# Kernel tuning notes

Hardware: AMD Instinct MI355X
Metric: run time of the kernel (lower is better)

The kernel has to match this reference:

```python
import jax, jax.numpy as jnp
import numpy as np

SIZE = 256


def setup_inputs() -> dict:
    key = jax.random.key(0)
    ks = jax.random.split(key, 16)
    B, T, S, V = 16, 128, 512, 32000
    s = SIZE
    inp = {}
    inp["inputs"] = jax.random.randint(ks[0], (B, T), 0, V)
    inp["features"] = jax.random.normal(ks[1], (B, S, 2 * s), dtype=jnp.float32)
    # parameters (PyTorch-style: y = x @ W.T + b)
    inp["emb"] = jax.random.normal(ks[2], (V, s), dtype=jnp.float32)
    inp["W_ih"] = jax.random.normal(ks[3], (4 * s, 2 * s), dtype=jnp.float32) * 0.05
    inp["W_hh"] = jax.random.normal(ks[4], (4 * s, s), dtype=jnp.float32) * 0.05
    inp["b_ih"] = jax.random.normal(ks[5], (4 * s,), dtype=jnp.float32) * 0.05
    inp["b_hh"] = jax.random.normal(ks[6], (4 * s,), dtype=jnp.float32) * 0.05
    inp["Wq"] = jax.random.normal(ks[7], (s, s), dtype=jnp.float32) * 0.05
    inp["bq"] = jax.random.normal(ks[8], (s,), dtype=jnp.float32) * 0.05
    inp["Wk"] = jax.random.normal(ks[9], (s, 2 * s), dtype=jnp.float32) * 0.05
    inp["bk"] = jax.random.normal(ks[10], (s,), dtype=jnp.float32) * 0.05
    inp["Wv"] = jax.random.normal(ks[11], (s, 2 * s), dtype=jnp.float32) * 0.05
    inp["bv"] = jax.random.normal(ks[12], (s,), dtype=jnp.float32) * 0.05
    inp["Wo"] = jax.random.normal(ks[13], (V, 2 * s), dtype=jnp.float32) * 0.05
    inp["bo"] = jax.random.normal(ks[14], (V,), dtype=jnp.float32) * 0.05
    return inp


def _decode(inputs, features, emb, W_ih, W_hh, b_ih, b_hh,
            Wq, bq, Wk, bk, Wv, bv, Wo, bo):
    B, T = inputs.shape
    s = emb.shape[1]
    embeddings = emb[inputs]                      # [B, T, s]
    # features are constant across timesteps -> hoist key/value projections
    keys = features @ Wk.T + bk                   # [B, S, s]
    values = features @ Wv.T + bv                 # [B, S, s]

    def step(carry, emb_t):
        h, c, context = carry
        x = jnp.concatenate([emb_t, context], axis=1)          # [B, 2s]
        gates = x @ W_ih.T + b_ih + h @ W_hh.T + b_hh          # [B, 4s]
        i, f, g, o = jnp.split(gates, 4, axis=1)               # PyTorch gate order
        i, f, o = jax.nn.sigmoid(i), jax.nn.sigmoid(f), jax.nn.sigmoid(o)
        g = jnp.tanh(g)
        c_new = f * c + i * g
        h_new = o * jnp.tanh(c_new)
        # attention
        query = h_new @ Wq.T + bq                              # [B, s]
        scores = jnp.einsum('bsd,bd->bs', keys, query)         # [B, S]
        weights = jax.nn.softmax(scores, axis=1)
        ctx = jnp.einsum('bsd,bs->bd', values, weights)        # [B, s]
        out = jnp.concatenate([h_new, ctx], axis=1) @ Wo.T + bo  # [B, V]
        return (h_new, c_new, ctx), out

    h0 = jnp.zeros((B, s), dtype=embeddings.dtype)
    c0 = jnp.zeros((B, s), dtype=embeddings.dtype)
    ctx0 = jnp.zeros((B, s), dtype=embeddings.dtype)
    _, outs = jax.lax.scan(step, (h0, c0, ctx0), jnp.swapaxes(embeddings, 0, 1))
    return jnp.swapaxes(outs, 0, 1)               # [B, T, V]


def reference(inputs, features, emb, W_ih, W_hh, b_ih, b_hh,
              Wq, bq, Wk, bk, Wv, bv, Wo, bo):
    return _decode(inputs, features, emb, W_ih, W_hh, b_ih, b_hh,
                   Wq, bq, Wk, bk, Wv, bv, Wo, bo)
```

## Files before the change

kernel.cpp:

```cpp
#include <hip/hip_runtime.h>
#include <hip/hip_fp16.h>

#define DEVI __device__ __forceinline__

typedef __attribute__((ext_vector_type(4))) float f32x4;
typedef __attribute__((ext_vector_type(8))) short bf16x8;
typedef __attribute__((ext_vector_type(8))) _Float16 f16x8;
typedef __attribute__((ext_vector_type(2))) _Float16 f16x2;
typedef unsigned long long ull;

DEVI ushort f2bf(float x) {
  union { float f; unsigned u; } v; v.f = x;
  unsigned r = v.u + 0x7fffu + ((v.u >> 16) & 1u);
  return (ushort)(r >> 16);
}
DEVI float bf2f(ushort b) {
  union { unsigned u; float f; } v; v.u = ((unsigned)b) << 16; return v.f;
}
DEVI unsigned packh2(float a, float b) {
  return ((unsigned)__half_as_ushort(__float2half(b)) << 16) |
         (unsigned)__half_as_ushort(__float2half(a));
}
DEVI float dot2(unsigned a, unsigned b, float c) {
#if __has_builtin(__builtin_amdgcn_fdot2)
  return __builtin_amdgcn_fdot2(__builtin_bit_cast(f16x2, a),
                                __builtin_bit_cast(f16x2, b), c, false);
#else
  f16x2 ha = __builtin_bit_cast(f16x2, a), hb = __builtin_bit_cast(f16x2, b);
  return c + (float)ha[0] * (float)hb[0] + (float)ha[1] * (float)hb[1];
#endif
}
DEVI float sigmoidf_(float x) { return 1.f / (1.f + __expf(-x)); }
DEVI float tanh_fast(float x) {
  float e = __expf(2.f * x);
  return 1.f - 2.f / (e + 1.f);
}

DEVI void gstore64(ull* p, ull v) {
  __hip_atomic_store(p, v, __ATOMIC_RELAXED, __HIP_MEMORY_SCOPE_AGENT);
}
DEVI ull gload64(const ull* p) {
  return __hip_atomic_load(p, __ATOMIC_RELAXED, __HIP_MEMORY_SCOPE_AGENT);
}

template<bool SPLIT, bool ABF16, bool BBF16>
__global__ __launch_bounds__(256)
void gemm_kernel(const void* __restrict__ A_, int lda, const int* __restrict__ Aidx,
                 const void* __restrict__ Bw_, int ldb,
                 const float* __restrict__ bias, float* __restrict__ C,
                 int N, int K)
{
  constexpr int BK  = SPLIT ? 32 : 64;
  constexpr int LDT = BK + 8;
  constexpr int NV  = (128 * BK / 4) / 256;

  __shared__ ushort Ah[128 * LDT];
  __shared__ ushort Bh[128 * LDT];
  __shared__ ushort Al[SPLIT ? 128 * LDT : 4];
  __shared__ ushort Bl[SPLIT ? 128 * LDT : 4];

  const int tid  = threadIdx.x;
  const int bm   = blockIdx.x * 128, bn = blockIdx.y * 128;
  const int lane = tid & 63, wave = tid >> 6;
  const int wr   = wave >> 1, wc = wave & 1;
  const int fr   = lane & 15, quad = lane >> 4;

  f32x4 acc[4][4] = {};

  for (int kt = 0; kt < K; kt += BK) {
    __syncthreads();
#pragma unroll
    for (int i = 0; i < NV; ++i) {
      int v   = i * 256 + tid;
      int row = v / (BK / 4);
      int c4  = (v % (BK / 4)) * 4;
      int arow = Aidx ? Aidx[bm + row] : (bm + row);
      if (ABF16) {
        const ushort* A = (const ushort*)A_;
        ushort4 h = *reinterpret_cast<const ushort4*>(A + (size_t)arow * lda + kt + c4);
        *reinterpret_cast<ushort4*>(&Ah[row * LDT + c4]) = h;
      } else {
        const float* A = (const float*)A_;
        const float4 x = *reinterpret_cast<const float4*>(A + (size_t)arow * lda + kt + c4);
        ushort4 h; h.x = f2bf(x.x); h.y = f2bf(x.y); h.z = f2bf(x.z); h.w = f2bf(x.w);
        *reinterpret_cast<ushort4*>(&Ah[row * LDT + c4]) = h;
        if (SPLIT) {
          ushort4 l;
          l.x = f2bf(x.x - bf2f(h.x)); l.y = f2bf(x.y - bf2f(h.y));
          l.z = f2bf(x.z - bf2f(h.z)); l.w = f2bf(x.w - bf2f(h.w));
          *reinterpret_cast<ushort4*>(&Al[row * LDT + c4]) = l;
        }
      }
    }
#pragma unroll
    for (int i = 0; i < NV; ++i) {
      int v   = i * 256 + tid;
      int row = v / (BK / 4);
      int c4  = (v % (BK / 4)) * 4;
      if (BBF16) {
        const ushort* B16 = (const ushort*)Bw_;
        ushort4 h = *reinterpret_cast<const ushort4*>(B16 + (size_t)(bn + row) * ldb + kt + c4);
        *reinterpret_cast<ushort4*>(&Bh[row * LDT + c4]) = h;
      } else {
        const float* Bw = (const float*)Bw_;
        const float4 x = *reinterpret_cast<const float4*>(Bw + (size_t)(bn + row) * ldb + kt + c4);
        ushort4 h; h.x = f2bf(x.x); h.y = f2bf(x.y); h.z = f2bf(x.z); h.w = f2bf(x.w);
        *reinterpret_cast<ushort4*>(&Bh[row * LDT + c4]) = h;
        if (SPLIT) {
          ushort4 l;
          l.x = f2bf(x.x - bf2f(h.x)); l.y = f2bf(x.y - bf2f(h.y));
          l.z = f2bf(x.z - bf2f(h.z)); l.w = f2bf(x.w - bf2f(h.w));
          *reinterpret_cast<ushort4*>(&Bl[row * LDT + c4]) = l;
        }
      }
    }
    __syncthreads();
#pragma unroll
    for (int ks = 0; ks < BK; ks += 32) {
      bf16x8 ah[4], bh[4];
#pragma unroll
      for (int i = 0; i < 4; ++i) {
        ah[i] = *reinterpret_cast<const bf16x8*>(&Ah[(wr * 64 + i * 16 + fr) * LDT + ks + quad * 8]);
        bh[i] = *reinterpret_cast<const bf16x8*>(&Bh[(wc * 64 + i * 16 + fr) * LDT + ks + quad * 8]);
      }
      if (SPLIT) {
        bf16x8 al[4], bl[4];
#pragma unroll
        for (int i = 0; i < 4; ++i) {
          al[i] = *reinterpret_cast<const bf16x8*>(&Al[(wr * 64 + i * 16 + fr) * LDT + ks + quad * 8]);
          bl[i] = *reinterpret_cast<const bf16x8*>(&Bl[(wc * 64 + i * 16 + fr) * LDT + ks + quad * 8]);
        }
#pragma unroll
        for (int i = 0; i < 4; ++i)
#pragma unroll
          for (int j = 0; j < 4; ++j) {
            acc[i][j] = __builtin_amdgcn_mfma_f32_16x16x32_bf16(ah[i], bh[j], acc[i][j], 0, 0, 0);
            acc[i][j] = __builtin_amdgcn_mfma_f32_16x16x32_bf16(ah[i], bl[j], acc[i][j], 0, 0, 0);
            acc[i][j] = __builtin_amdgcn_mfma_f32_16x16x32_bf16(al[i], bh[j], acc[i][j], 0, 0, 0);
          }
      } else {
#pragma unroll
        for (int i = 0; i < 4; ++i)
#pragma unroll
          for (int j = 0; j < 4; ++j)
            acc[i][j] = __builtin_amdgcn_mfma_f32_16x16x32_bf16(ah[i], bh[j], acc[i][j], 0, 0, 0);
      }
    }
  }
#pragma unroll
  for (int i = 0; i < 4; ++i)
#pragma unroll
    for (int j = 0; j < 4; ++j)
#pragma unroll
      for (int r = 0; r < 4; ++r) {
        int m = bm + wr * 64 + i * 16 + quad * 4 + r;
        int n = bn + wc * 64 + j * 16 + fr;
        float vv = acc[i][j][r];
        if (bias) vv += bias[n];
        C[(size_t)m * N + n] = vv;
      }
}

__global__ void prep_kernel(const float* __restrict__ Wq, float* __restrict__ WqT,
                            const float* __restrict__ b_ih, const float* __restrict__ b_hh,
                            float* __restrict__ bsum)
{
  int idx = blockIdx.x * 256 + threadIdx.x;
  if (idx < 65536) {
    int e = idx >> 8, d = idx & 255;
    WqT[idx] = Wq[d * 256 + e];
  } else if (idx < 66560) {
    int n = idx - 65536;
    bsum[n] = b_ih[n] + b_hh[n];
  }
}

__global__ void sb_kernel(const float* __restrict__ keys, const float* __restrict__ bq,
                          float* __restrict__ sb)
{
  int row  = blockIdx.x * 4 + (threadIdx.x >> 6);
  int lane = threadIdx.x & 63;
  const float* kr = keys + (size_t)row * 256;
  float acc = kr[lane] * bq[lane] + kr[64 + lane] * bq[64 + lane]
            + kr[128 + lane] * bq[128 + lane] + kr[192 + lane] * bq[192 + lane];
#pragma unroll
  for (int off = 1; off < 64; off <<= 1) acc += __shfl_xor(acc, off);
  if (lane == 0) sb[row] = acc;
}

__global__ void cvt_kernel(const float* __restrict__ src, ushort* __restrict__ dst, int n4)
{
  int i = blockIdx.x * 256 + threadIdx.x;
  if (i < n4) {
    float4 x = reinterpret_cast<const float4*>(src)[i];
    ushort4 h; h.x = f2bf(x.x); h.y = f2bf(x.y); h.z = f2bf(x.z); h.w = f2bf(x.w);
    reinterpret_cast<ushort4*>(dst)[i] = h;
  }
}

struct ScanSmem2 {
  unsigned k2p[64][131];
  unsigned vtp[256][35];
  unsigned xw[288];
  unsigned psp[32];
  float Erow[128];
  float gout[128];
  float ml[8][2];
  float cpart[4][128][2];
  float sc[8][64];
  float sbs[64];
};

DEVI int xwi(int w) { return (w >> 6) * 72 + (w & 63); }

__global__ __launch_bounds__(512, 1)
void scan2_kernel(const float* __restrict__ E, const float* __restrict__ K2g,
                  const float* __restrict__ sbg, const float* __restrict__ valg,
                  const float* __restrict__ W_ih, const float* __restrict__ W_hh,
                  ushort* __restrict__ hcb16,
                  ull* __restrict__ Hx,
                  ull* __restrict__ Px)
{
  extern __shared__ char smraw[];
  ScanSmem2& sm = *reinterpret_cast<ScanSmem2*>(smraw);
  const int g = blockIdx.x, tid = threadIdx.x;
  const int b = g >> 3, ss = g & 7;

  for (int idx = tid; idx < 64 * 128; idx += 512) {
    int j = idx >> 7, i = idx & 127;
    const float* src = K2g + (size_t)(b * 512 + ss * 64 + j) * 256 + 2 * i;
    sm.k2p[j][i] = packh2(src[0], src[1]);
  }
  for (int idx = tid; idx < 256 * 32; idx += 512) {
    int e = idx >> 5, jp = idx & 31;
    float v0 = valg[(size_t)(b * 512 + ss * 64 + 2 * jp) * 256 + e];
    float v1 = valg[(size_t)(b * 512 + ss * 64 + 2 * jp + 1) * 256 + e];
    sm.vtp[e][jp] = packh2(v0, v1);
  }
  if (tid < 64) sm.sbs[tid] = sbg[b * 512 + ss * 64 + tid];
  for (int i = tid; i < 288; i += 512) sm.xw[i] = 0;

  const int r  = tid >> 2, h4 = tid & 3;
  const int grow = (r >> 5) * 256 + ss * 32 + (r & 31);
  const float* wsrc = (h4 < 2)
      ? (W_ih + (size_t)grow * 512 + 256 + h4 * 128)
      : (W_hh + (size_t)grow * 256 + (h4 - 2) * 128);
  unsigned wreg[64];
#pragma unroll
  for (int i = 0; i < 32; ++i) {
    float4 w4 = reinterpret_cast<const float4*>(wsrc)[i];
    wreg[2 * i]     = packh2(w4.x, w4.y);
    wreg[2 * i + 1] = packh2(w4.z, w4.w);
  }

  float c_reg = 0.f;
  __syncthreads();

  const size_t hxb = (size_t)b * 128;
  const size_t pxb = (size_t)b * (8 * 130);

  for (int t = 0; t <= 128; ++t) {
    float epf = 0.f;
    if (t < 128 && tid < 128)
      epf = E[(size_t)(b * 128 + t) * 1024 + (tid >> 5) * 256 + ss * 32 + (tid & 31)];

    float accg = 0.f;
    if (t > 0) {
      const unsigned tag = (unsigned)t;
      const ull* PxP = Px + (size_t)((t - 1) & 1) * (16 * 8 * 130) + pxb;
      const int e2 = tid & 127, q = tid >> 7;
      const ull* p1 = &PxP[(2 * q) * 130 + e2];
      const ull* p2 = &PxP[(2 * q + 1) * 130 + e2];
      ull w1 = gload64(p1), w2 = gload64(p2);
      const ull* pm = &PxP[(tid >> 1) * 130 + 128 + (tid & 1)];
      ull wm = (tid < 16) ? gload64(pm) : 0;

      if (h4 >= 2) {
        const unsigned* xsrc = sm.xw + h4 * 72;
#pragma unroll
        for (int i = 0; i < 16; ++i) {
          uint4 xv = *reinterpret_cast<const uint4*>(xsrc + 4 * i);
          accg = dot2(wreg[4 * i + 0], xv.x, accg);
          accg = dot2(wreg[4 * i + 1], xv.y, accg);
          accg = dot2(wreg[4 * i + 2], xv.z, accg);
          accg = dot2(wreg[4 * i + 3], xv.w, accg);
        }
      }

      if (tid < 16) {
        while ((unsigned)(wm >> 32) != tag) { __builtin_amdgcn_s_sleep(1); wm = gload64(pm); }
        sm.ml[tid >> 1][tid & 1] = __uint_as_float((unsigned)wm);
      }
      while ((unsigned)(w1 >> 32) != tag) { __builtin_amdgcn_s_sleep(1); w1 = gload64(p1); }
      while ((unsigned)(w2 >> 32) != tag) { __builtin_amdgcn_s_sleep(1); w2 = gload64(p2); }
      __syncthreads();
      float M = sm.ml[0][0];
#pragma unroll
      for (int s3 = 1; s3 < 8; ++s3) M = fmaxf(M, sm.ml[s3][0]);
      float L = 0.f;
#pragma unroll
      for (int s3 = 0; s3 < 8; ++s3) L += sm.ml[s3][1] * __expf(sm.ml[s3][0] - M);
      float rcpL = 1.f / L;
      float wf0 = __expf(sm.ml[2 * q][0] - M);
      float wf1 = __expf(sm.ml[2 * q + 1][0] - M);
      f16x2 x1 = __builtin_bit_cast(f16x2, (unsigned)w1);
      f16x2 x2 = __builtin_bit_cast(f16x2, (unsigned)w2);
      sm.cpart[q][e2][0] = wf0 * (float)x1[0] + wf1 * (float)x2[0];
      sm.cpart[q][e2][1] = wf0 * (float)x1[1] + wf1 * (float)x2[1];
      __syncthreads();
      if (tid < 128) {
        float c0 = (sm.cpart[0][tid][0] + sm.cpart[1][tid][0]
                  + sm.cpart[2][tid][0] + sm.cpart[3][tid][0]) * rcpL;
        float c1 = (sm.cpart[0][tid][1] + sm.cpart[1][tid][1]
                  + sm.cpart[2][tid][1] + sm.cpart[3][tid][1]) * rcpL;
        sm.xw[xwi(tid)] = packh2(c0, c1);
        ushort* dst = hcb16 + (size_t)(b * 128 + (t - 1)) * 512 + 256 + 2 * tid;
        dst[0] = f2bf(c0); dst[1] = f2bf(c1);
      }
    }
    if (t == 128) break;
    if (tid < 128) sm.Erow[tid] = epf;
    __syncthreads();

    if (t > 0 && h4 < 2) {
      const unsigned* xsrc = sm.xw + h4 * 72;
#pragma unroll
      for (int i = 0; i < 16; ++i) {
        uint4 xv = *reinterpret_cast<const uint4*>(xsrc + 4 * i);
        accg = dot2(wreg[4 * i + 0], xv.x, accg);
        accg = dot2(wreg[4 * i + 1], xv.y, accg);
        accg = dot2(wreg[4 * i + 2], xv.z, accg);
        accg = dot2(wreg[4 * i + 3], xv.w, accg);
      }
    }
    accg += __shfl_xor(accg, 1);
    accg += __shfl_xor(accg, 2);
    if (h4 == 0) sm.gout[r] = accg;
    __syncthreads();

    if (tid < 32) {
      float gi = sm.gout[tid]      + sm.Erow[tid];
      float gf = sm.gout[32 + tid] + sm.Erow[32 + tid];
      float gg = sm.gout[64 + tid] + sm.Erow[64 + tid];
      float go = sm.gout[96 + tid] + sm.Erow[96 + tid];
      float iv = sigmoidf_(gi), fv = sigmoidf_(gf), ov = sigmoidf_(go);
      float gv = tanh_fast(gg);
      c_reg = fv * c_reg + iv * gv;
      float hn = ov * tanh_fast(c_reg);
      hcb16[(size_t)(b * 128 + t) * 512 + ss * 32 + tid] = f2bf(hn);
      float ho = __shfl_xor(hn, 1);
      if (!(tid & 1)) {
        unsigned pk = packh2(hn, ho);
        int w = ss * 16 + (tid >> 1);
        sm.xw[xwi(128 + w)] = pk;
        gstore64(&Hx[(size_t)(t & 1) * 2048 + hxb + w],
                 ((ull)(unsigned)(t + 1) << 32) | pk);
      }
    }
    if (tid < 128 && (tid >> 4) != ss) {
      const ull* hp = &Hx[(size_t)(t & 1) * 2048 + hxb + tid];
      ull w = gload64(hp);
      while ((unsigned)(w >> 32) != (unsigned)(t + 1)) {
        __builtin_amdgcn_s_sleep(1); w = gload64(hp);
      }
      sm.xw[xwi(128 + tid)] = (unsigned)w;
    }
    __syncthreads();

    {
      const int j = tid & 63, qq = tid >> 6;
      float acc2 = 0.f;
#pragma unroll
      for (int i = 0; i < 16; ++i)
        acc2 = dot2(sm.k2p[j][qq * 16 + i], sm.xw[xwi(128 + qq * 16 + i)], acc2);
      sm.sc[qq][j] = acc2;
    }
    __syncthreads();
    if (tid < 64) {
      float s = sm.sc[0][tid] + sm.sc[1][tid] + sm.sc[2][tid] + sm.sc[3][tid]
              + sm.sc[4][tid] + sm.sc[5][tid] + sm.sc[6][tid] + sm.sc[7][tid]
              + sm.sbs[tid];
      float mx = s;
#pragma unroll
      for (int off = 1; off < 64; off <<= 1) mx = fmaxf(mx, __shfl_xor(mx, off));
      float p = __expf(s - mx);
      float ls = p;
#pragma unroll
      for (int off = 1; off < 64; off <<= 1) ls += __shfl_xor(ls, off);
      if (tid == 0) {
        ull tg = (ull)(unsigned)(t + 1) << 32;
        ull* PxS = Px + (size_t)(t & 1) * (16 * 8 * 130) + pxb + ss * 130;
        gstore64(&PxS[128], tg | __float_as_uint(mx));
        gstore64(&PxS[129], tg | __float_as_uint(ls));
      }
      float ph = __shfl_xor(p, 1);
      if (!(tid & 1)) sm.psp[tid >> 1] = packh2(p, ph);
    }
    __syncthreads();
    if (tid < 256) {
      float acc2 = 0.f;
#pragma unroll
      for (int jp = 0; jp < 32; ++jp) acc2 = dot2(sm.psp[jp], sm.vtp[tid][jp], acc2);
      float ao = __shfl_xor(acc2, 1);
      if (!(tid & 1)) {
        ull* PxS = Px + (size_t)(t & 1) * (16 * 8 * 130) + pxb + ss * 130;
        gstore64(&PxS[tid >> 1], ((ull)(unsigned)(t + 1) << 32) | packh2(acc2, ao));
      }
    }
  }
}

extern "C" void kernel_launch(void* const* d_in, const int* in_sizes, int n_in,
                              void* d_out, int out_size, void* d_ws, size_t ws_size,
                              hipStream_t stream)
{
  const int*   inputs   = (const int*)  d_in[0];
  const float* features = (const float*)d_in[1];
  const float* emb      = (const float*)d_in[2];
  const float* W_ih     = (const float*)d_in[3];
  const float* W_hh     = (const float*)d_in[4];
  const float* b_ih     = (const float*)d_in[5];
  const float* b_hh     = (const float*)d_in[6];
  const float* Wq       = (const float*)d_in[7];
  const float* bq       = (const float*)d_in[8];
  const float* Wk       = (const float*)d_in[9];
  const float* bk       = (const float*)d_in[10];
  const float* Wv       = (const float*)d_in[11];
  const float* bv       = (const float*)d_in[12];
  const float* Wo       = (const float*)d_in[13];
  const float* bo       = (const float*)d_in[14];
  float* out = (float*)d_out;

  char* ws = (char*)d_ws;
  size_t off = 0;
  auto alloc = [&](size_t bytes) -> char* {
    char* p = ws + off;
    off += (bytes + 255) & ~size_t(255);
    return p;
  };
  float*  keys  = (float*) alloc((size_t)8192 * 256 * 4);
  float*  vals  = (float*) alloc((size_t)8192 * 256 * 4);
  float*  K2    = (float*) alloc((size_t)8192 * 256 * 4);
  float*  E     = (float*) alloc((size_t)2048 * 1024 * 4);
  float*  WqT   = (float*) alloc((size_t)256 * 256 * 4);
  float*  sb    = (float*) alloc((size_t)8192 * 4);
  float*  bsum  = (float*) alloc((size_t)1024 * 4);
  ushort* hcb16 = (ushort*)alloc((size_t)2048 * 512 * 2);
  ull*    Hx    = (ull*)   alloc((size_t)2 * 16 * 128 * 8);
  ull*    Px    = (ull*)   alloc((size_t)2 * 16 * 8 * 130 * 8);

  const size_t woBytes = (size_t)32000 * 512 * 2;
  ushort* Wo16 = nullptr;
  if (off + woBytes + 256 <= ws_size) Wo16 = (ushort*)alloc(woBytes);

  hipMemsetAsync(Hx, 0, (size_t)2 * 16 * 128 * 8, stream);
  hipMemsetAsync(Px, 0, (size_t)2 * 16 * 8 * 130 * 8, stream);

  prep_kernel<<<260, 256, 0, stream>>>(Wq, WqT, b_ih, b_hh, bsum);

  gemm_kernel<true, false, false><<<dim3(64, 2), 256, 0, stream>>>(features, 512, nullptr, Wk, 512, bk, keys, 256, 512);
  gemm_kernel<true, false, false><<<dim3(64, 2), 256, 0, stream>>>(features, 512, nullptr, Wv, 512, bv, vals, 256, 512);
  gemm_kernel<true, false, false><<<dim3(64, 2), 256, 0, stream>>>(keys, 256, nullptr, WqT, 256, nullptr, K2, 256, 256);
  sb_kernel<<<2048, 256, 0, stream>>>(keys, bq, sb);
  gemm_kernel<true, false, false><<<dim3(16, 8), 256, 0, stream>>>(emb, 256, inputs, W_ih, 512, bsum, E, 1024, 256);

  if (Wo16) cvt_kernel<<<16000, 256, 0, stream>>>(Wo, Wo16, 32000 * 512 / 4);

  hipFuncSetAttribute(reinterpret_cast<const void*>(scan2_kernel),
                      hipFuncAttributeMaxDynamicSharedMemorySize, (int)sizeof(ScanSmem2));
  scan2_kernel<<<128, 512, sizeof(ScanSmem2), stream>>>(E, K2, sb, vals, W_ih, W_hh,
                                                        hcb16, Hx, Px);

  if (Wo16)
    gemm_kernel<false, true, true><<<dim3(16, 250), 256, 0, stream>>>(hcb16, 512, nullptr, Wo16, 512, bo, out, 32000, 512);
  else
    gemm_kernel<false, true, false><<<dim3(16, 250), 256, 0, stream>>>(hcb16, 512, nullptr, Wo, 512, bo, out, 32000, 512);
}
```

Measured before the change: 1.401 ms.

## Fold query weights into key projection, fuse KV GEMM, swizzle output GEMM blocks

```diff
diff --git a/kernel.cpp b/kernel.cpp
--- a/kernel.cpp
+++ b/kernel.cpp
@@ -43,7 +43,7 @@
   return __hip_atomic_load(p, __ATOMIC_RELAXED, __HIP_MEMORY_SCOPE_AGENT);
 }
 
-template<bool SPLIT, bool ABF16, bool BBF16>
+template<bool SPLIT, bool ABF16, bool BBF16, bool SWZ>
 __global__ __launch_bounds__(256)
 void gemm_kernel(const void* __restrict__ A_, int lda, const int* __restrict__ Aidx,
                  const void* __restrict__ Bw_, int ldb,
@@ -59,8 +59,19 @@
   __shared__ ushort Al[SPLIT ? 128 * LDT : 4];
   __shared__ ushort Bl[SPLIT ? 128 * LDT : 4];
 
+  int bm, bn;
+  if (SWZ) {
+    int bid = blockIdx.x;
+    int r8 = bid & 7, k = bid >> 3;
+    int x = k & 15, yhi = k >> 4;
+    int y = yhi * 8 + r8;
+    if (y >= 250) return;
+    bm = x * 128; bn = y * 128;
+  } else {
+    bm = blockIdx.x * 128; bn = blockIdx.y * 128;
+  }
+
   const int tid  = threadIdx.x;
-  const int bm   = blockIdx.x * 128, bn = blockIdx.y * 128;
   const int lane = tid & 63, wave = tid >> 6;
   const int wr   = wave >> 1, wc = wave & 1;
   const int fr   = lane & 15, quad = lane >> 4;
@@ -161,31 +172,75 @@
       }
 }
 
-__global__ void prep_kernel(const float* __restrict__ Wq, float* __restrict__ WqT,
-                            const float* __restrict__ b_ih, const float* __restrict__ b_hh,
-                            float* __restrict__ bsum)
+__global__ __launch_bounds__(256)
+void prep2_kernel(const float* __restrict__ Wk, const float* __restrict__ Wq,
+                  const float* __restrict__ Wv, const float* __restrict__ bk,
+                  const float* __restrict__ bq, const float* __restrict__ b_ih,
+                  const float* __restrict__ b_hh, const float* __restrict__ bv,
+                  float* __restrict__ Bcomb, float* __restrict__ bias512,
+                  float* __restrict__ bsum, float* __restrict__ wkbq,
+                  float* __restrict__ cbbv)
 {
-  int idx = blockIdx.x * 256 + threadIdx.x;
-  if (idx < 65536) {
-    int e = idx >> 8, d = idx & 255;
-    WqT[idx] = Wq[d * 256 + e];
-  } else if (idx < 66560) {
-    int n = idx - 65536;
-    bsum[n] = b_ih[n] + b_hh[n];
-  }
-}
-
-__global__ void sb_kernel(const float* __restrict__ keys, const float* __restrict__ bq,
-                          float* __restrict__ sb)
+  __shared__ float col[256];
+  __shared__ float red[256];
+  const int blk = blockIdx.x, tid = threadIdx.x;
+  if (blk < 256) {
+    const int e = blk;
+    float cv = Wq[(size_t)tid * 256 + e];
+    col[tid] = cv;
+    red[tid] = bk[tid] * cv;
+    __syncthreads();
+    float a0 = 0.f, a1 = 0.f;
+    for (int d = 0; d < 256; ++d) {
+      float wq = col[d];
+      a0 = fmaf(Wk[(size_t)d * 512 + tid], wq, a0);
+      a1 = fmaf(Wk[(size_t)d * 512 + 256 + tid], wq, a1);
+    }
+    Bcomb[(size_t)(256 + e) * 512 + tid] = a0;
+    Bcomb[(size_t)(256 + e) * 512 + 256 + tid] = a1;
+    if (tid == 0) {
+      float s = 0.f;
+      for (int d = 0; d < 256; ++d) s += red[d];
+      bias512[256 + e] = s;
+    }
+  } else {
+    for (int i = tid; i < 256 * 512 / 4; i += 256)
+      reinterpret_cast<float4*>(Bcomb)[i] = reinterpret_cast<const float4*>(Wv)[i];
+    bias512[tid] = bv[tid];
+    for (int i = tid; i < 1024; i += 256) bsum[i] = b_ih[i] + b_hh[i];
+    float bqv = bq[tid];
+    col[tid] = bqv;
+    red[tid] = bk[tid] * bqv;
+    __syncthreads();
+    float a0 = 0.f, a1 = 0.f;
+    for (int d = 0; d < 256; ++d) {
+      float v = col[d];
+      a0 = fmaf(Wk[(size_t)d * 512 + tid], v, a0);
+      a1 = fmaf(Wk[(size_t)d * 512 + 256 + tid], v, a1);
+    }
+    wkbq[tid] = a0; wkbq[256 + tid] = a1;
+    if (tid == 0) {
+      float s = 0.f;
+      for (int d = 0; d < 256; ++d) s += red[d];
+      cbbv[0] = s;
+    }
+  }
+}
+
+__global__ void sb2_kernel(const float* __restrict__ features,
+                           const float* __restrict__ wkbq,
+                           const float* __restrict__ cbbv,
+                           float* __restrict__ sb)
 {
   int row  = blockIdx.x * 4 + (threadIdx.x >> 6);
   int lane = threadIdx.x & 63;
-  const float* kr = keys + (size_t)row * 256;
-  float acc = kr[lane] * bq[lane] + kr[64 + lane] * bq[64 + lane]
-            + kr[128 + lane] * bq[128 + lane] + kr[192 + lane] * bq[192 + lane];
+  const float* fr = features + (size_t)row * 512;
+  float acc = 0.f;
+#pragma unroll
+  for (int k = 0; k < 8; ++k) acc = fmaf(fr[k * 64 + lane], wkbq[k * 64 + lane], acc);
 #pragma unroll
   for (int off = 1; off < 64; off <<= 1) acc += __shfl_xor(acc, off);
-  if (lane == 0) sb[row] = acc;
+  if (lane == 0) sb[row] = acc + cbbv[0];
 }
 
 __global__ void cvt_kernel(const float* __restrict__ src, ushort* __restrict__ dst, int n4)
@@ -206,7 +261,7 @@
   float Erow[128];
   float gout[128];
   float ml[8][2];
-  float cpart[4][128][2];
+  float part[8][130];
   float sc[8][64];
   float sbs[64];
 };
@@ -214,8 +269,8 @@
 DEVI int xwi(int w) { return (w >> 6) * 72 + (w & 63); }
 
 __global__ __launch_bounds__(512, 1)
-void scan2_kernel(const float* __restrict__ E, const float* __restrict__ K2g,
-                  const float* __restrict__ sbg, const float* __restrict__ valg,
+void scan2_kernel(const float* __restrict__ E, const float* __restrict__ KV2,
+                  const float* __restrict__ sbg,
                   const float* __restrict__ W_ih, const float* __restrict__ W_hh,
                   ushort* __restrict__ hcb16,
                   ull* __restrict__ Hx,
@@ -228,13 +283,13 @@
 
   for (int idx = tid; idx < 64 * 128; idx += 512) {
     int j = idx >> 7, i = idx & 127;
-    const float* src = K2g + (size_t)(b * 512 + ss * 64 + j) * 256 + 2 * i;
+    const float* src = KV2 + (size_t)(b * 512 + ss * 64 + j) * 512 + 256 + 2 * i;
     sm.k2p[j][i] = packh2(src[0], src[1]);
   }
   for (int idx = tid; idx < 256 * 32; idx += 512) {
     int e = idx >> 5, jp = idx & 31;
-    float v0 = valg[(size_t)(b * 512 + ss * 64 + 2 * jp) * 256 + e];
-    float v1 = valg[(size_t)(b * 512 + ss * 64 + 2 * jp + 1) * 256 + e];
+    float v0 = KV2[(size_t)(b * 512 + ss * 64 + 2 * jp) * 512 + e];
+    float v1 = KV2[(size_t)(b * 512 + ss * 64 + 2 * jp + 1) * 512 + e];
     sm.vtp[e][jp] = packh2(v0, v1);
   }
   if (tid < 64) sm.sbs[tid] = sbg[b * 512 + ss * 64 + tid];
@@ -305,32 +360,47 @@
       float wf1 = __expf(sm.ml[2 * q + 1][0] - M);
       f16x2 x1 = __builtin_bit_cast(f16x2, (unsigned)w1);
       f16x2 x2 = __builtin_bit_cast(f16x2, (unsigned)w2);
-      sm.cpart[q][e2][0] = wf0 * (float)x1[0] + wf1 * (float)x2[0];
-      sm.cpart[q][e2][1] = wf0 * (float)x1[1] + wf1 * (float)x2[1];
+      float2 pw0; pw0.x = wf0 * (float)x1[0] + wf1 * (float)x2[0];
+      float2 pw1; pw1.x = wf0 * (float)x1[1] + wf1 * (float)x2[1];
+      sm.part[2 * q][e2]     = pw0.x;
+      sm.part[2 * q + 1][e2] = pw1.x;
       __syncthreads();
-      if (tid < 128) {
-        float c0 = (sm.cpart[0][tid][0] + sm.cpart[1][tid][0]
-                  + sm.cpart[2][tid][0] + sm.cpart[3][tid][0]) * rcpL;
-        float c1 = (sm.cpart[0][tid][1] + sm.cpart[1][tid][1]
-                  + sm.cpart[2][tid][1] + sm.cpart[3][tid][1]) * rcpL;
-        sm.xw[xwi(tid)] = packh2(c0, c1);
-        ushort* dst = hcb16 + (size_t)(b * 128 + (t - 1)) * 512 + 256 + 2 * tid;
-        dst[0] = f2bf(c0); dst[1] = f2bf(c1);
+      {
+        const int l = tid & 63;
+        float2 f0[8];
+#pragma unroll
+        for (int s4 = 0; s4 < 8; ++s4)
+          f0[s4] = *reinterpret_cast<const float2*>(&sm.part[s4][2 * l]);
+        float c00 = (f0[0].x + f0[2].x + f0[4].x + f0[6].x) * rcpL;
+        float c01 = (f0[1].x + f0[3].x + f0[5].x + f0[7].x) * rcpL;
+        float c10 = (f0[0].y + f0[2].y + f0[4].y + f0[6].y) * rcpL;
+        float c11 = (f0[1].y + f0[3].y + f0[5].y + f0[7].y) * rcpL;
+        sm.xw[xwi(2 * l)]     = packh2(c00, c01);
+        sm.xw[xwi(2 * l + 1)] = packh2(c10, c11);
+        if (tid < 64) {
+          ushort4 st;
+          st.x = f2bf(c00); st.y = f2bf(c01); st.z = f2bf(c10); st.w = f2bf(c11);
+          *reinterpret_cast<ushort4*>(
+              hcb16 + (size_t)(b * 128 + (t - 1)) * 512 + 256 + 4 * l) = st;
+        }
       }
     }
     if (t == 128) break;
     if (tid < 128) sm.Erow[tid] = epf;
-    __syncthreads();
-
-    if (t > 0 && h4 < 2) {
-      const unsigned* xsrc = sm.xw + h4 * 72;
-#pragma unroll
-      for (int i = 0; i < 16; ++i) {
-        uint4 xv = *reinterpret_cast<const uint4*>(xsrc + 4 * i);
-        accg = dot2(wreg[4 * i + 0], xv.x, accg);
-        accg = dot2(wreg[4 * i + 1], xv.y, accg);
-        accg = dot2(wreg[4 * i + 2], xv.z, accg);
-        accg = dot2(wreg[4 * i + 3], xv.w, accg);
+
+    if (t > 0) {
+      asm volatile("s_waitcnt lgkmcnt(0)" ::: "memory");
+      __builtin_amdgcn_sched_barrier(0);
+      if (h4 < 2) {
+        const unsigned* xsrc = sm.xw + h4 * 72;
+#pragma unroll
+        for (int i = 0; i < 16; ++i) {
+          uint4 xv = *reinterpret_cast<const uint4*>(xsrc + 4 * i);
+          accg = dot2(wreg[4 * i + 0], xv.x, accg);
+          accg = dot2(wreg[4 * i + 1], xv.y, accg);
+          accg = dot2(wreg[4 * i + 2], xv.z, accg);
+          accg = dot2(wreg[4 * i + 3], xv.w, accg);
+        }
       }
     }
     accg += __shfl_xor(accg, 1);
@@ -438,13 +508,14 @@
     off += (bytes + 255) & ~size_t(255);
     return p;
   };
-  float*  keys  = (float*) alloc((size_t)8192 * 256 * 4);
-  float*  vals  = (float*) alloc((size_t)8192 * 256 * 4);
-  float*  K2    = (float*) alloc((size_t)8192 * 256 * 4);
+  float*  KV2   = (float*) alloc((size_t)8192 * 512 * 4);
   float*  E     = (float*) alloc((size_t)2048 * 1024 * 4);
-  float*  WqT   = (float*) alloc((size_t)256 * 256 * 4);
+  float*  Bcomb = (float*) alloc((size_t)512 * 512 * 4);
+  float*  bias512 = (float*)alloc((size_t)512 * 4);
   float*  sb    = (float*) alloc((size_t)8192 * 4);
   float*  bsum  = (float*) alloc((size_t)1024 * 4);
+  float*  wkbq  = (float*) alloc((size_t)512 * 4);
+  float*  cbbv  = (float*) alloc((size_t)64 * 4);
   ushort* hcb16 = (ushort*)alloc((size_t)2048 * 512 * 2);
   ull*    Hx    = (ull*)   alloc((size_t)2 * 16 * 128 * 8);
   ull*    Px    = (ull*)   alloc((size_t)2 * 16 * 8 * 130 * 8);
@@ -456,23 +527,26 @@
   hipMemsetAsync(Hx, 0, (size_t)2 * 16 * 128 * 8, stream);
   hipMemsetAsync(Px, 0, (size_t)2 * 16 * 8 * 130 * 8, stream);
 
-  prep_kernel<<<260, 256, 0, stream>>>(Wq, WqT, b_ih, b_hh, bsum);
-
-  gemm_kernel<true, false, false><<<dim3(64, 2), 256, 0, stream>>>(features, 512, nullptr, Wk, 512, bk, keys, 256, 512);
-  gemm_kernel<true, false, false><<<dim3(64, 2), 256, 0, stream>>>(features, 512, nullptr, Wv, 512, bv, vals, 256, 512);
-  gemm_kernel<true, false, false><<<dim3(64, 2), 256, 0, stream>>>(keys, 256, nullptr, WqT, 256, nullptr, K2, 256, 256);
-  sb_kernel<<<2048, 256, 0, stream>>>(keys, bq, sb);
-  gemm_kernel<true, false, false><<<dim3(16, 8), 256, 0, stream>>>(emb, 256, inputs, W_ih, 512, bsum, E, 1024, 256);
+  prep2_kernel<<<257, 256, 0, stream>>>(Wk, Wq, Wv, bk, bq, b_ih, b_hh, bv,
+                                        Bcomb, bias512, bsum, wkbq, cbbv);
+
+  gemm_kernel<true, false, false, false><<<dim3(64, 4), 256, 0, stream>>>(
+      features, 512, nullptr, Bcomb, 512, bias512, KV2, 512, 512);
+  sb2_kernel<<<2048, 256, 0, stream>>>(features, wkbq, cbbv, sb);
+  gemm_kernel<true, false, false, false><<<dim3(16, 8), 256, 0, stream>>>(
+      emb, 256, inputs, W_ih, 512, bsum, E, 1024, 256);
 
   if (Wo16) cvt_kernel<<<16000, 256, 0, stream>>>(Wo, Wo16, 32000 * 512 / 4);
 
   hipFuncSetAttribute(reinterpret_cast<const void*>(scan2_kernel),
                       hipFuncAttributeMaxDynamicSharedMemorySize, (int)sizeof(ScanSmem2));
-  scan2_kernel<<<128, 512, sizeof(ScanSmem2), stream>>>(E, K2, sb, vals, W_ih, W_hh,
+  scan2_kernel<<<128, 512, sizeof(ScanSmem2), stream>>>(E, KV2, sb, W_ih, W_hh,
                                                         hcb16, Hx, Px);
 
   if (Wo16)
-    gemm_kernel<false, true, true><<<dim3(16, 250), 256, 0, stream>>>(hcb16, 512, nullptr, Wo16, 512, bo, out, 32000, 512);
+    gemm_kernel<false, true, true, true><<<4096, 256, 0, stream>>>(
+        hcb16, 512, nullptr, Wo16, 512, bo, out, 32000, 512);
   else
-    gemm_kernel<false, true, false><<<dim3(16, 250), 256, 0, stream>>>(hcb16, 512, nullptr, Wo, 512, bo, out, 32000, 512);
-}
+    gemm_kernel<false, true, false, true><<<4096, 256, 0, stream>>>(
+        hcb16, 512, nullptr, Wo, 512, bo, out, 32000, 512);
+}
```

Measured after the change: 1.427 ms. No clear change (+1.9%).
